# Kernel optimization log

Hardware: AMD Instinct MI355X
Metric: run time of the kernel (lower is better)

## Reference

```python
import jax, jax.numpy as jnp
import numpy as np

N, K, M, D = 50000, 32, 50000, 128  # dst nodes, neighbors, src nodes, hidden_dim


def setup_inputs() -> dict:
    key = jax.random.key(0)
    k1, k2, k3, k4 = jax.random.split(key, 4)
    nei = jax.random.randint(k1, (N, K), 0, M, dtype=jnp.int64)
    h = jax.random.normal(k2, (M, D), dtype=jnp.float32)
    h_refer = jax.random.normal(k3, (N, D), dtype=jnp.float32)
    # xavier_normal_ on (1, 2D) with gain=1.414: std = gain*sqrt(2/(1+2D))
    std = 1.414 * np.sqrt(2.0 / (1 + 2 * D))
    att = jax.random.normal(k4, (1, 2 * D), dtype=jnp.float32) * std
    return {"nei": nei, "h": h, "h_refer": h_refer, "att": att}


def reference(nei, h, h_refer, att):
    # gather neighbor embeddings: [N, K, D]
    nei_emb = h[nei]
    # split att so we never materialize the concatenated [N, K, 2D] tensor:
    # cat([h_refer, nei_emb], -1) @ att.T == h_refer @ att_ref + nei_emb @ att_nei
    att_ref = att[0, :D]   # [D]
    att_nei = att[0, D:]   # [D]
    scores = (h_refer @ att_ref)[:, None] + jnp.einsum("nkd,d->nk", nei_emb, att_nei)  # [N, K]
    scores = jax.nn.leaky_relu(scores, negative_slope=0.01)
    w = jax.nn.softmax(scores, axis=1)  # softmax over neighbors
    # weighted sum over neighbors -> [N, D]
    return jnp.einsum("nk,nkd->nd", w, nei_emb)
```

## Files before the change

### kernel.cpp

```cpp
#include <hip/hip_runtime.h>

typedef unsigned int uint32;
typedef unsigned long long uint64;
typedef unsigned short ushort_t;
typedef _Float16 h2_t __attribute__((ext_vector_type(2)));
typedef float  f32x2 __attribute__((ext_vector_type(2)));
typedef float  f32x4 __attribute__((ext_vector_type(4)));
typedef uint32 u32x2 __attribute__((ext_vector_type(2)));

#define KNEI 32
#define DIM 128
#define WPB 4
#define RPW 2

enum { SRC_BF16 = 0, SRC_F16 = 1, SRC_F32 = 2 };

__device__ __forceinline__ float bflo(uint32 u) {
    union { uint32 u; float f; } c; c.u = u << 16; return c.f;
}
__device__ __forceinline__ float bfhi(uint32 u) {
    union { uint32 u; float f; } c; c.u = u & 0xffff0000u; return c.f;
}
__device__ __forceinline__ uint32 pack_bf16_rne(float a, float b) {
    union { float f; uint32 u; } x, y; x.f = a; y.f = b;
    uint32 ua = (x.u + 0x7fffu + ((x.u >> 16) & 1u)) >> 16;
    uint32 ub = (y.u + 0x7fffu + ((y.u >> 16) & 1u)) >> 16;
    return (ua & 0xffffu) | (ub << 16);
}
__device__ __forceinline__ uint32 pack_f16(float a, float b) {
    union { h2_t h; uint32 u; } c;
    c.h.x = (_Float16)a; c.h.y = (_Float16)b;
    return c.u;
}
__device__ __forceinline__ h2_t as_h2(uint32 u) {
    union { uint32 u; h2_t h; } c; c.u = u; return c.h;
}

__device__ __forceinline__ bool probe_bf16(const void* h, int lane) {
    const uint32 hs = ((const uint32*)h)[lane];
    const uint32 e  = (hs >> 7) & 0xFFu;
    const bool  tb  = (e >= 90u) && (e <= 140u);
    return (__ballot(tb) == ~0ull);
}

template<int SRC>
__device__ __forceinline__ void process_row(
    const uint4* ev, const float* an, float base,
    void* __restrict__ outv, size_t n, int lane, int r4, int c)
{
    constexpr bool F32 = (SRC != SRC_BF16);

    float s[8];
    #pragma unroll
    for (int it = 0; it < 8; ++it) {
        const uint4 e = ev[it];
        if constexpr (SRC == SRC_BF16) {
            s[it] = bflo(e.x) * an[0] + bfhi(e.x) * an[1]
                  + bflo(e.y) * an[2] + bfhi(e.y) * an[3]
                  + bflo(e.z) * an[4] + bfhi(e.z) * an[5]
                  + bflo(e.w) * an[6] + bfhi(e.w) * an[7];
        } else {
            const h2_t e0 = as_h2(e.x), e1 = as_h2(e.y), e2 = as_h2(e.z), e3 = as_h2(e.w);
            const float t0 = fmaf((float)e0.x, an[0],
                             fmaf((float)e0.y, an[1],
                             fmaf((float)e1.x, an[2], (float)e1.y * an[3])));
            const float t1 = fmaf((float)e2.x, an[4],
                             fmaf((float)e2.y, an[5],
                             fmaf((float)e3.x, an[6], (float)e3.y * an[7])));
            s[it] = t0 + t1;
        }
    }
    #pragma unroll
    for (int off = 1; off <= 8; off <<= 1) {
        #pragma unroll
        for (int it = 0; it < 8; ++it)
            s[it] += __shfl_xor(s[it], off, 64);
    }
    #pragma unroll
    for (int it = 0; it < 8; ++it) {
        const float v = base + s[it];
        s[it] = (v > 0.f) ? v : 0.01f * v;
    }

    float m = s[0];
    #pragma unroll
    for (int it = 1; it < 8; ++it) m = fmaxf(m, s[it]);
    m = fmaxf(m, __shfl_xor(m, 16, 64));
    m = fmaxf(m, __shfl_xor(m, 32, 64));

    float w[8];
    float sum = 0.f;
    #pragma unroll
    for (int it = 0; it < 8; ++it) { w[it] = __expf(s[it] - m); sum += w[it]; }
    sum += __shfl_xor(sum, 16, 64);
    sum += __shfl_xor(sum, 32, 64);
    const float inv = 1.0f / sum;

    float acc[8] = {0.f, 0.f, 0.f, 0.f, 0.f, 0.f, 0.f, 0.f};
    #pragma unroll
    for (int it = 0; it < 8; ++it) {
        const float wk = w[it] * inv;
        const uint4 e = ev[it];
        if constexpr (SRC == SRC_BF16) {
            acc[0] = fmaf(wk, bflo(e.x), acc[0]);
            acc[1] = fmaf(wk, bfhi(e.x), acc[1]);
            acc[2] = fmaf(wk, bflo(e.y), acc[2]);
            acc[3] = fmaf(wk, bfhi(e.y), acc[3]);
            acc[4] = fmaf(wk, bflo(e.z), acc[4]);
            acc[5] = fmaf(wk, bfhi(e.z), acc[5]);
            acc[6] = fmaf(wk, bflo(e.w), acc[6]);
            acc[7] = fmaf(wk, bfhi(e.w), acc[7]);
        } else {
            const h2_t e0 = as_h2(e.x), e1 = as_h2(e.y), e2 = as_h2(e.z), e3 = as_h2(e.w);
            acc[0] = fmaf(wk, (float)e0.x, acc[0]);
            acc[1] = fmaf(wk, (float)e0.y, acc[1]);
            acc[2] = fmaf(wk, (float)e1.x, acc[2]);
            acc[3] = fmaf(wk, (float)e1.y, acc[3]);
            acc[4] = fmaf(wk, (float)e2.x, acc[4]);
            acc[5] = fmaf(wk, (float)e2.y, acc[5]);
            acc[6] = fmaf(wk, (float)e3.x, acc[6]);
            acc[7] = fmaf(wk, (float)e3.y, acc[7]);
        }
    }
    #pragma unroll
    for (int d = 0; d < 8; ++d) acc[d] += __shfl_xor(acc[d], 16, 64);
    #pragma unroll
    for (int d = 0; d < 8; ++d) acc[d] += __shfl_xor(acc[d], 32, 64);

    const float q0a = (r4 & 2) ? acc[4] : acc[0];
    const float q0b = (r4 & 2) ? acc[5] : acc[1];
    const float q1a = (r4 & 2) ? acc[6] : acc[2];
    const float q1b = (r4 & 2) ? acc[7] : acc[3];
    const float o0 = (r4 & 1) ? q1a : q0a;
    const float o1 = (r4 & 1) ? q1b : q0b;

    if (F32) {
        f32x2 o; o.x = o0; o.y = o1;
        __builtin_nontemporal_store(o, (f32x2*)((float*)outv + n * DIM) + c * 4 + r4);
    } else {
        __builtin_nontemporal_store(pack_bf16_rne(o0, o1),
            (uint32*)((ushort_t*)outv + n * DIM) + c * 4 + r4);
    }
}

template<int SRC>
__device__ __forceinline__ void run_two(
    const void* __restrict__ hsv, const void* __restrict__ hrv,
    const void* __restrict__ attv, void* __restrict__ outv,
    const void* __restrict__ neiv, bool i64, int Mrows,
    int n0, bool valid2, int lane)
{
    constexpr bool F32 = (SRC != SRC_BF16);
    const int r4 = lane >> 4;
    const int c  = lane & 15;

    const size_t ebase = (size_t)n0 * KNEI;
    const int esel = valid2 ? lane : (lane & 31);
    int idxv;
    if (i64) idxv = (int)__builtin_nontemporal_load((const long long*)neiv + ebase + esel);
    else     idxv = __builtin_nontemporal_load((const int*)neiv + ebase + esel);
    idxv = min(max(idxv, 0), Mrows - 1);

    int rows_a[8], rows_b[8];
    #pragma unroll
    for (int it = 0; it < 8; ++it) {
        rows_a[it] = __shfl(idxv, it * 4 + r4, 64);
        rows_b[it] = __shfl(idxv, 32 + it * 4 + r4, 64);
    }

    uint4 eva[8], evb[8];
    #pragma unroll
    for (int it = 0; it < 8; ++it) {
        if constexpr (SRC == SRC_F32) {
            const float4* sp = (const float4*)hsv + ((size_t)rows_a[it] << 5) + c * 2;
            const float4 p0 = sp[0], p1 = sp[1];
            eva[it].x = pack_f16(p0.x, p0.y);
            eva[it].y = pack_f16(p0.z, p0.w);
            eva[it].z = pack_f16(p1.x, p1.y);
            eva[it].w = pack_f16(p1.z, p1.w);
        } else {
            eva[it] = *((const uint4*)hsv + ((size_t)rows_a[it] << 4) + c);
        }
    }
    #pragma unroll
    for (int it = 0; it < 8; ++it) {
        if constexpr (SRC == SRC_F32) {
            const float4* sp = (const float4*)hsv + ((size_t)rows_b[it] << 5) + c * 2;
            const float4 p0 = sp[0], p1 = sp[1];
            evb[it].x = pack_f16(p0.x, p0.y);
            evb[it].y = pack_f16(p0.z, p0.w);
            evb[it].z = pack_f16(p1.x, p1.y);
            evb[it].w = pack_f16(p1.z, p1.w);
        } else {
            evb[it] = *((const uint4*)hsv + ((size_t)rows_b[it] << 4) + c);
        }
    }

    const int r2 = lane >> 5;
    const int l5 = lane & 31;
    const size_t brow = (size_t)n0 + (valid2 ? r2 : 0);
    float bsum;
    if (F32) {
        const f32x4 hp = __builtin_nontemporal_load(
            (const f32x4*)((const float*)hrv + brow * DIM) + l5);
        const f32x4 ap = *((const f32x4*)attv + l5);
        bsum = hp.x * ap.x + hp.y * ap.y + hp.z * ap.z + hp.w * ap.w;
    } else {
        const u32x2 hu = __builtin_nontemporal_load(
            (const u32x2*)((const ushort_t*)hrv + brow * DIM) + l5);
        const u32x2 au = *((const u32x2*)attv + l5);
        bsum = bflo(hu.x) * bflo(au.x) + bfhi(hu.x) * bfhi(au.x)
             + bflo(hu.y) * bflo(au.y) + bfhi(hu.y) * bfhi(au.y);
    }
    #pragma unroll
    for (int off = 1; off <= 16; off <<= 1)
        bsum += __shfl_xor(bsum, off, 64);
    const float baseA = __shfl(bsum, 0, 64);
    const float baseB = __shfl(bsum, 32, 64);

    float an[8];
    if (F32) {
        const float4* ap = (const float4*)((const float*)attv + DIM + c * 8);
        const float4 p0 = ap[0], p1 = ap[1];
        an[0] = p0.x; an[1] = p0.y; an[2] = p0.z; an[3] = p0.w;
        an[4] = p1.x; an[5] = p1.y; an[6] = p1.z; an[7] = p1.w;
    } else {
        const uint4 au = *((const uint4*)((const ushort_t*)attv + DIM) + c);
        an[0] = bflo(au.x); an[1] = bfhi(au.x); an[2] = bflo(au.y); an[3] = bfhi(au.y);
        an[4] = bflo(au.z); an[5] = bfhi(au.z); an[6] = bflo(au.w); an[7] = bfhi(au.w);
    }

    process_row<SRC>(eva, an, baseA, outv, (size_t)n0, lane, r4, c);
    if (valid2)
        process_row<SRC>(evb, an, baseB, outv, (size_t)n0 + 1, lane, r4, c);
}

__global__ __launch_bounds__(256) void gat_kernel(
    const void* __restrict__ nei, const void* __restrict__ h,
    const void* __restrict__ h_refer, const void* __restrict__ att,
    void* __restrict__ out, const void* __restrict__ hf16,
    int N, int Mrows, int use_ws)
{
    const int tid  = threadIdx.x;
    const int lane = tid & 63;
    const int n0   = (blockIdx.x * WPB + (tid >> 6)) * RPW;

    const bool is_bf16 = probe_bf16(h, lane);
    const uint32 nhi = ((const uint32*)nei)[2 * lane + 1];
    const bool  i64  = (__ballot(nhi == 0u) == ~0ull);

    if (n0 >= N) return;
    const bool valid2 = (n0 + 1 < N);

    if (is_bf16)     run_two<SRC_BF16>(h,    h_refer, att, out, nei, i64, Mrows, n0, valid2, lane);
    else if (use_ws) run_two<SRC_F16 >(hf16, h_refer, att, out, nei, i64, Mrows, n0, valid2, lane);
    else             run_two<SRC_F32 >(h,    h_refer, att, out, nei, i64, Mrows, n0, valid2, lane);
}

__global__ __launch_bounds__(256) void conv_kernel(
    const void* __restrict__ h, uint4* __restrict__ ws, long long ngroups)
{
    if (probe_bf16(h, threadIdx.x & 63)) return;
    const long long i = (long long)blockIdx.x * 256 + threadIdx.x;
    if (i >= ngroups) return;
    const f32x4* sp = (const f32x4*)h + i * 2;
    const f32x4 p0 = __builtin_nontemporal_load(sp);
    const f32x4 p1 = __builtin_nontemporal_load(sp + 1);
    uint4 o;
    o.x = pack_f16(p0.x, p0.y);
    o.y = pack_f16(p0.z, p0.w);
    o.z = pack_f16(p1.x, p1.y);
    o.w = pack_f16(p1.z, p1.w);
    ws[i] = o;
}

extern "C" void kernel_launch(void* const* d_in, const int* in_sizes, int n_in,
                              void* d_out, int out_size, void* d_ws, size_t ws_size,
                              hipStream_t stream) {
    const int N = out_size / DIM;
    const int M = in_sizes[1] / DIM;

    const size_t need = (size_t)M * DIM * sizeof(ushort_t);
    const int use_ws = (d_ws != nullptr && ws_size >= need) ? 1 : 0;

    if (use_ws) {
        const long long ngroups = (long long)M * (DIM / 8);
        dim3 cg((unsigned)((ngroups + 255) / 256)), cb(256);
        conv_kernel<<<cg, cb, 0, stream>>>(d_in[1], (uint4*)d_ws, ngroups);
    }

    const int rows_per_block = WPB * RPW;
    dim3 grid((N + rows_per_block - 1) / rows_per_block), block(64 * WPB);
    gat_kernel<<<grid, block, 0, stream>>>(d_in[0], d_in[1], d_in[2], d_in[3],
                                           d_out, d_ws, N, M, use_ws);
}
```

Baseline: 147.5 us.

## Prefetch second row's neighbor gathers into LDS via global_load_lds while processing first

For the bf16/f16 paths, the second destination row's neighbor rows are fetched asynchronously into per-wave LDS buffers with global_load_lds, so the first row's softmax and accumulation can overlap with those loads. The register footprint for the second row's gather is reduced, and launch bounds now request higher occupancy. The final cross-lane reduction is also restructured into a reduce-scatter that halves the number of shuffles. The cost is 32KB of LDS per block, which may limit occupancy, plus an explicit vmcnt(0) wait.

```diff
diff --git a/kernel.cpp b/kernel.cpp
--- a/kernel.cpp
+++ b/kernel.cpp
@@ -12,6 +12,7 @@
 #define DIM 128
 #define WPB 4
 #define RPW 2
+#define WAVE_LDS 8192
 
 enum { SRC_BF16 = 0, SRC_F16 = 1, SRC_F32 = 2 };
 
@@ -36,6 +37,13 @@
     union { uint32 u; h2_t h; } c; c.u = u; return c.h;
 }
 
+__device__ __forceinline__ void prefetch16(const void* g, void* l) {
+    __builtin_amdgcn_global_load_lds(
+        (const __attribute__((address_space(1))) void*)g,
+        (__attribute__((address_space(3))) void*)l,
+        16, 0, 0);
+}
+
 __device__ __forceinline__ bool probe_bf16(const void* h, int lane) {
     const uint32 hs = ((const uint32*)h)[lane];
     const uint32 e  = (hs >> 7) & 0xFFu;
@@ -44,32 +52,55 @@
 }
 
 template<int SRC>
-__device__ __forceinline__ void process_row(
-    const uint4* ev, const float* an, float base,
-    void* __restrict__ outv, size_t n, int lane, int r4, int c)
+__device__ __forceinline__ float dot8(const uint4 e, const float* an) {
+    if constexpr (SRC == SRC_BF16) {
+        return bflo(e.x) * an[0] + bfhi(e.x) * an[1]
+             + bflo(e.y) * an[2] + bfhi(e.y) * an[3]
+             + bflo(e.z) * an[4] + bfhi(e.z) * an[5]
+             + bflo(e.w) * an[6] + bfhi(e.w) * an[7];
+    } else {
+        const h2_t e0 = as_h2(e.x), e1 = as_h2(e.y), e2 = as_h2(e.z), e3 = as_h2(e.w);
+        const float t0 = fmaf((float)e0.x, an[0],
+                         fmaf((float)e0.y, an[1],
+                         fmaf((float)e1.x, an[2], (float)e1.y * an[3])));
+        const float t1 = fmaf((float)e2.x, an[4],
+                         fmaf((float)e2.y, an[5],
+                         fmaf((float)e3.x, an[6], (float)e3.y * an[7])));
+        return t0 + t1;
+    }
+}
+
+template<int SRC>
+__device__ __forceinline__ void acc8(float* acc, float wk, const uint4 e) {
+    if constexpr (SRC == SRC_BF16) {
+        acc[0] = fmaf(wk, bflo(e.x), acc[0]);
+        acc[1] = fmaf(wk, bfhi(e.x), acc[1]);
+        acc[2] = fmaf(wk, bflo(e.y), acc[2]);
+        acc[3] = fmaf(wk, bfhi(e.y), acc[3]);
+        acc[4] = fmaf(wk, bflo(e.z), acc[4]);
+        acc[5] = fmaf(wk, bfhi(e.z), acc[5]);
+        acc[6] = fmaf(wk, bflo(e.w), acc[6]);
+        acc[7] = fmaf(wk, bfhi(e.w), acc[7]);
+    } else {
+        const h2_t e0 = as_h2(e.x), e1 = as_h2(e.y), e2 = as_h2(e.z), e3 = as_h2(e.w);
+        acc[0] = fmaf(wk, (float)e0.x, acc[0]);
+        acc[1] = fmaf(wk, (float)e0.y, acc[1]);
+        acc[2] = fmaf(wk, (float)e1.x, acc[2]);
+        acc[3] = fmaf(wk, (float)e1.y, acc[3]);
+        acc[4] = fmaf(wk, (float)e2.x, acc[4]);
+        acc[5] = fmaf(wk, (float)e2.y, acc[5]);
+        acc[6] = fmaf(wk, (float)e3.x, acc[6]);
+        acc[7] = fmaf(wk, (float)e3.y, acc[7]);
+    }
+}
+
+template<int SRC>
+__device__ __forceinline__ f32x2 process_row(
+    const uint4* ev, const float* an, float base, int r4)
 {
-    constexpr bool F32 = (SRC != SRC_BF16);
-
     float s[8];
     #pragma unroll
-    for (int it = 0; it < 8; ++it) {
-        const uint4 e = ev[it];
-        if constexpr (SRC == SRC_BF16) {
-            s[it] = bflo(e.x) * an[0] + bfhi(e.x) * an[1]
-                  + bflo(e.y) * an[2] + bfhi(e.y) * an[3]
-                  + bflo(e.z) * an[4] + bfhi(e.z) * an[5]
-                  + bflo(e.w) * an[6] + bfhi(e.w) * an[7];
-        } else {
-            const h2_t e0 = as_h2(e.x), e1 = as_h2(e.y), e2 = as_h2(e.z), e3 = as_h2(e.w);
-            const float t0 = fmaf((float)e0.x, an[0],
-                             fmaf((float)e0.y, an[1],
-                             fmaf((float)e1.x, an[2], (float)e1.y * an[3])));
-            const float t1 = fmaf((float)e2.x, an[4],
-                             fmaf((float)e2.y, an[5],
-                             fmaf((float)e3.x, an[6], (float)e3.y * an[7])));
-            s[it] = t0 + t1;
-        }
-    }
+    for (int it = 0; it < 8; ++it) s[it] = dot8<SRC>(ev[it], an);
     #pragma unroll
     for (int off = 1; off <= 8; off <<= 1) {
         #pragma unroll
@@ -82,65 +113,43 @@
         s[it] = (v > 0.f) ? v : 0.01f * v;
     }
 
-    float m = s[0];
-    #pragma unroll
-    for (int it = 1; it < 8; ++it) m = fmaxf(m, s[it]);
+    float m = fmaxf(fmaxf(fmaxf(s[0], s[1]), fmaxf(s[2], s[3])),
+                    fmaxf(fmaxf(s[4], s[5]), fmaxf(s[6], s[7])));
     m = fmaxf(m, __shfl_xor(m, 16, 64));
     m = fmaxf(m, __shfl_xor(m, 32, 64));
 
     float w[8];
-    float sum = 0.f;
-    #pragma unroll
-    for (int it = 0; it < 8; ++it) { w[it] = __expf(s[it] - m); sum += w[it]; }
+    #pragma unroll
+    for (int it = 0; it < 8; ++it) w[it] = __expf(s[it] - m);
+    float sum = ((w[0] + w[1]) + (w[2] + w[3])) + ((w[4] + w[5]) + (w[6] + w[7]));
     sum += __shfl_xor(sum, 16, 64);
     sum += __shfl_xor(sum, 32, 64);
     const float inv = 1.0f / sum;
 
     float acc[8] = {0.f, 0.f, 0.f, 0.f, 0.f, 0.f, 0.f, 0.f};
     #pragma unroll
-    for (int it = 0; it < 8; ++it) {
-        const float wk = w[it] * inv;
-        const uint4 e = ev[it];
-        if constexpr (SRC == SRC_BF16) {
-            acc[0] = fmaf(wk, bflo(e.x), acc[0]);
-            acc[1] = fmaf(wk, bfhi(e.x), acc[1]);
-            acc[2] = fmaf(wk, bflo(e.y), acc[2]);
-            acc[3] = fmaf(wk, bfhi(e.y), acc[3]);
-            acc[4] = fmaf(wk, bflo(e.z), acc[4]);
-            acc[5] = fmaf(wk, bfhi(e.z), acc[5]);
-            acc[6] = fmaf(wk, bflo(e.w), acc[6]);
-            acc[7] = fmaf(wk, bfhi(e.w), acc[7]);
-        } else {
-            const h2_t e0 = as_h2(e.x), e1 = as_h2(e.y), e2 = as_h2(e.z), e3 = as_h2(e.w);
-            acc[0] = fmaf(wk, (float)e0.x, acc[0]);
-            acc[1] = fmaf(wk, (float)e0.y, acc[1]);
-            acc[2] = fmaf(wk, (float)e1.x, acc[2]);
-            acc[3] = fmaf(wk, (float)e1.y, acc[3]);
-            acc[4] = fmaf(wk, (float)e2.x, acc[4]);
-            acc[5] = fmaf(wk, (float)e2.y, acc[5]);
-            acc[6] = fmaf(wk, (float)e3.x, acc[6]);
-            acc[7] = fmaf(wk, (float)e3.y, acc[7]);
-        }
-    }
-    #pragma unroll
-    for (int d = 0; d < 8; ++d) acc[d] += __shfl_xor(acc[d], 16, 64);
-    #pragma unroll
-    for (int d = 0; d < 8; ++d) acc[d] += __shfl_xor(acc[d], 32, 64);
-
-    const float q0a = (r4 & 2) ? acc[4] : acc[0];
-    const float q0b = (r4 & 2) ? acc[5] : acc[1];
-    const float q1a = (r4 & 2) ? acc[6] : acc[2];
-    const float q1b = (r4 & 2) ? acc[7] : acc[3];
-    const float o0 = (r4 & 1) ? q1a : q0a;
-    const float o1 = (r4 & 1) ? q1b : q0b;
-
-    if (F32) {
-        f32x2 o; o.x = o0; o.y = o1;
-        __builtin_nontemporal_store(o, (f32x2*)((float*)outv + n * DIM) + c * 4 + r4);
-    } else {
-        __builtin_nontemporal_store(pack_bf16_rne(o0, o1),
-            (uint32*)((ushort_t*)outv + n * DIM) + c * 4 + r4);
-    }
+    for (int it = 0; it < 8; ++it)
+        acc8<SRC>(acc, w[it] * inv, ev[it]);
+
+    const bool b1 = (r4 & 2) != 0;
+    const bool b0 = (r4 & 1) != 0;
+    float t[4];
+    #pragma unroll
+    for (int j = 0; j < 4; ++j) {
+        const float keep = b1 ? acc[4 + j] : acc[j];
+        const float send = b1 ? acc[j]     : acc[4 + j];
+        t[j] = keep + __shfl_xor(send, 32, 64);
+    }
+    f32x2 o;
+    {
+        const float k0 = b0 ? t[2] : t[0];
+        const float s0 = b0 ? t[0] : t[2];
+        o.x = k0 + __shfl_xor(s0, 16, 64);
+        const float k1 = b0 ? t[3] : t[1];
+        const float s1 = b0 ? t[1] : t[3];
+        o.y = k1 + __shfl_xor(s1, 16, 64);
+    }
+    return o;
 }
 
 template<int SRC>
@@ -148,75 +157,35 @@
     const void* __restrict__ hsv, const void* __restrict__ hrv,
     const void* __restrict__ attv, void* __restrict__ outv,
     const void* __restrict__ neiv, bool i64, int Mrows,
-    int n0, bool valid2, int lane)
+    size_t n0, bool valid2, int lane, char* wbase)
 {
     constexpr bool F32 = (SRC != SRC_BF16);
     const int r4 = lane >> 4;
     const int c  = lane & 15;
 
-    const size_t ebase = (size_t)n0 * KNEI;
+    const size_t ebase = n0 * KNEI;
     const int esel = valid2 ? lane : (lane & 31);
     int idxv;
     if (i64) idxv = (int)__builtin_nontemporal_load((const long long*)neiv + ebase + esel);
     else     idxv = __builtin_nontemporal_load((const int*)neiv + ebase + esel);
     idxv = min(max(idxv, 0), Mrows - 1);
 
-    int rows_a[8], rows_b[8];
-    #pragma unroll
-    for (int it = 0; it < 8; ++it) {
-        rows_a[it] = __shfl(idxv, it * 4 + r4, 64);
-        rows_b[it] = __shfl(idxv, 32 + it * 4 + r4, 64);
-    }
-
-    uint4 eva[8], evb[8];
-    #pragma unroll
-    for (int it = 0; it < 8; ++it) {
-        if constexpr (SRC == SRC_F32) {
-            const float4* sp = (const float4*)hsv + ((size_t)rows_a[it] << 5) + c * 2;
-            const float4 p0 = sp[0], p1 = sp[1];
-            eva[it].x = pack_f16(p0.x, p0.y);
-            eva[it].y = pack_f16(p0.z, p0.w);
-            eva[it].z = pack_f16(p1.x, p1.y);
-            eva[it].w = pack_f16(p1.z, p1.w);
-        } else {
-            eva[it] = *((const uint4*)hsv + ((size_t)rows_a[it] << 4) + c);
-        }
-    }
-    #pragma unroll
-    for (int it = 0; it < 8; ++it) {
-        if constexpr (SRC == SRC_F32) {
-            const float4* sp = (const float4*)hsv + ((size_t)rows_b[it] << 5) + c * 2;
-            const float4 p0 = sp[0], p1 = sp[1];
-            evb[it].x = pack_f16(p0.x, p0.y);
-            evb[it].y = pack_f16(p0.z, p0.w);
-            evb[it].z = pack_f16(p1.x, p1.y);
-            evb[it].w = pack_f16(p1.z, p1.w);
-        } else {
-            evb[it] = *((const uint4*)hsv + ((size_t)rows_b[it] << 4) + c);
-        }
-    }
-
-    const int r2 = lane >> 5;
-    const int l5 = lane & 31;
-    const size_t brow = (size_t)n0 + (valid2 ? r2 : 0);
-    float bsum;
+    const int r2 = lane >> 5, l5 = lane & 31;
+    const size_t brow = n0 + (valid2 ? (size_t)r2 : 0);
+    float hb[4], ab[4];
     if (F32) {
         const f32x4 hp = __builtin_nontemporal_load(
             (const f32x4*)((const float*)hrv + brow * DIM) + l5);
         const f32x4 ap = *((const f32x4*)attv + l5);
-        bsum = hp.x * ap.x + hp.y * ap.y + hp.z * ap.z + hp.w * ap.w;
+        hb[0] = hp.x; hb[1] = hp.y; hb[2] = hp.z; hb[3] = hp.w;
+        ab[0] = ap.x; ab[1] = ap.y; ab[2] = ap.z; ab[3] = ap.w;
     } else {
         const u32x2 hu = __builtin_nontemporal_load(
             (const u32x2*)((const ushort_t*)hrv + brow * DIM) + l5);
         const u32x2 au = *((const u32x2*)attv + l5);
-        bsum = bflo(hu.x) * bflo(au.x) + bfhi(hu.x) * bfhi(au.x)
-             + bflo(hu.y) * bflo(au.y) + bfhi(hu.y) * bfhi(au.y);
-    }
-    #pragma unroll
-    for (int off = 1; off <= 16; off <<= 1)
-        bsum += __shfl_xor(bsum, off, 64);
-    const float baseA = __shfl(bsum, 0, 64);
-    const float baseB = __shfl(bsum, 32, 64);
+        hb[0] = bflo(hu.x); hb[1] = bfhi(hu.x); hb[2] = bflo(hu.y); hb[3] = bfhi(hu.y);
+        ab[0] = bflo(au.x); ab[1] = bfhi(au.x); ab[2] = bflo(au.y); ab[3] = bfhi(au.y);
+    }
 
     float an[8];
     if (F32) {
@@ -230,31 +199,103 @@
         an[4] = bflo(au.z); an[5] = bfhi(au.z); an[6] = bflo(au.w); an[7] = bfhi(au.w);
     }
 
-    process_row<SRC>(eva, an, baseA, outv, (size_t)n0, lane, r4, c);
-    if (valid2)
-        process_row<SRC>(evb, an, baseB, outv, (size_t)n0 + 1, lane, r4, c);
-}
-
-__global__ __launch_bounds__(256) void gat_kernel(
+    int rows_a[8], rows_b[8];
+    #pragma unroll
+    for (int it = 0; it < 8; ++it) {
+        rows_a[it] = __shfl(idxv, it * 4 + r4, 64);
+        rows_b[it] = __shfl(idxv, 32 + it * 4 + r4, 64);
+    }
+
+    uint4 evA[8];
+    #pragma unroll
+    for (int it = 0; it < 8; ++it) {
+        if constexpr (SRC == SRC_F32) {
+            const float4* sp = (const float4*)hsv + ((size_t)rows_a[it] << 5) + c * 2;
+            const float4 p0 = sp[0], p1 = sp[1];
+            evA[it].x = pack_f16(p0.x, p0.y);
+            evA[it].y = pack_f16(p0.z, p0.w);
+            evA[it].z = pack_f16(p1.x, p1.y);
+            evA[it].w = pack_f16(p1.z, p1.w);
+        } else {
+            evA[it] = *((const uint4*)hsv + ((size_t)rows_a[it] << 4) + c);
+        }
+    }
+
+    if constexpr (SRC != SRC_F32) {
+        #pragma unroll
+        for (int it = 0; it < 8; ++it)
+            prefetch16((const uint4*)hsv + ((size_t)rows_b[it] << 4) + c,
+                       wbase + it * 1024);
+    }
+
+    float bsum = hb[0] * ab[0] + hb[1] * ab[1] + hb[2] * ab[2] + hb[3] * ab[3];
+    #pragma unroll
+    for (int off = 1; off <= 16; off <<= 1)
+        bsum += __shfl_xor(bsum, off, 64);
+    const float baseA = __shfl(bsum, 0, 64);
+    const float baseB = __shfl(bsum, 32, 64);
+
+    const f32x2 oA = process_row<SRC>(evA, an, baseA, r4);
+
+    f32x2 oB;
+    if constexpr (SRC == SRC_F32) {
+        uint4 evB[8];
+        #pragma unroll
+        for (int it = 0; it < 8; ++it) {
+            const float4* sp = (const float4*)hsv + ((size_t)rows_b[it] << 5) + c * 2;
+            const float4 p0 = sp[0], p1 = sp[1];
+            evB[it].x = pack_f16(p0.x, p0.y);
+            evB[it].y = pack_f16(p0.z, p0.w);
+            evB[it].z = pack_f16(p1.x, p1.y);
+            evB[it].w = pack_f16(p1.z, p1.w);
+        }
+        oB = process_row<SRC>(evB, an, baseB, r4);
+    } else {
+        __builtin_amdgcn_sched_barrier(0);
+        asm volatile("s_waitcnt vmcnt(0)" ::: "memory");
+        uint4 evB[8];
+        #pragma unroll
+        for (int it = 0; it < 8; ++it)
+            evB[it] = *(const uint4*)(wbase + it * 1024 + lane * 16);
+        oB = process_row<SRC>(evB, an, baseB, r4);
+    }
+
+    if (F32) {
+        __builtin_nontemporal_store(oA, (f32x2*)((float*)outv + n0 * DIM) + c * 4 + r4);
+        if (valid2)
+            __builtin_nontemporal_store(oB, (f32x2*)((float*)outv + (n0 + 1) * DIM) + c * 4 + r4);
+    } else {
+        __builtin_nontemporal_store(pack_bf16_rne(oA.x, oA.y),
+            (uint32*)((ushort_t*)outv + n0 * DIM) + c * 4 + r4);
+        if (valid2)
+            __builtin_nontemporal_store(pack_bf16_rne(oB.x, oB.y),
+                (uint32*)((ushort_t*)outv + (n0 + 1) * DIM) + c * 4 + r4);
+    }
+}
+
+__global__ __launch_bounds__(256, 8) void gat_kernel(
     const void* __restrict__ nei, const void* __restrict__ h,
     const void* __restrict__ h_refer, const void* __restrict__ att,
     void* __restrict__ out, const void* __restrict__ hf16,
     int N, int Mrows, int use_ws)
 {
+    __shared__ __align__(16) char smem[WPB * WAVE_LDS];
     const int tid  = threadIdx.x;
     const int lane = tid & 63;
-    const int n0   = (blockIdx.x * WPB + (tid >> 6)) * RPW;
+    const int wave = tid >> 6;
+    const size_t n0 = ((size_t)blockIdx.x * WPB + wave) * RPW;
 
     const bool is_bf16 = probe_bf16(h, lane);
     const uint32 nhi = ((const uint32*)nei)[2 * lane + 1];
     const bool  i64  = (__ballot(nhi == 0u) == ~0ull);
 
-    if (n0 >= N) return;
-    const bool valid2 = (n0 + 1 < N);
-
-    if (is_bf16)     run_two<SRC_BF16>(h,    h_refer, att, out, nei, i64, Mrows, n0, valid2, lane);
-    else if (use_ws) run_two<SRC_F16 >(hf16, h_refer, att, out, nei, i64, Mrows, n0, valid2, lane);
-    else             run_two<SRC_F32 >(h,    h_refer, att, out, nei, i64, Mrows, n0, valid2, lane);
+    if (n0 >= (size_t)N) return;
+    const bool valid2 = (n0 + 1 < (size_t)N);
+    char* wbase = smem + wave * WAVE_LDS;
+
+    if (is_bf16)     run_two<SRC_BF16>(h,    h_refer, att, out, nei, i64, Mrows, n0, valid2, lane, wbase);
+    else if (use_ws) run_two<SRC_F16 >(hf16, h_refer, att, out, nei, i64, Mrows, n0, valid2, lane, wbase);
+    else             run_two<SRC_F32 >(h,    h_refer, att, out, nei, i64, Mrows, n0, valid2, lane, wbase);
 }
 
 __global__ __launch_bounds__(256) void conv_kernel(
```

Result: slower. 166.3 us (+12.7%).
